# Kernel tuning notes

Hardware: AMD Instinct MI355X
Metric: run time of the kernel (lower is better)

Reference implementation:

```python
import jax, jax.numpy as jnp
import numpy as np

N = 100000; NFEAT = 256; NHID = 128; NCLASS = 40; DEG = 16; E = N * DEG
L = 2; AH = 16; ALPHA = 0.2; LP_ALPHA = 0.5


def setup_inputs() -> dict:
    key = jax.random.key(0)
    ks = jax.random.split(key, 12)
    s = 0.05
    x = jax.random.normal(ks[0], (N, NFEAT), jnp.float32)
    row = jnp.repeat(jnp.arange(N), DEG)                       # each node has DEG out-edges
    col = jax.random.randint(ks[1], (E,), 0, N)
    edges = jnp.stack([row, col])                              # [2, E]
    degree = jax.random.uniform(ks[2], (N, 1), jnp.float32, 0.5, 1.5)
    label = jax.random.uniform(ks[3], (N, NCLASS), jnp.float32)
    return {
        "x": x, "edges": edges, "degree": degree, "iftrain": 0, "label": label,
        "lb_w": jax.random.normal(ks[4], (NHID, NFEAT)) * s,
        "lb_b": jnp.zeros((NHID,)),
        "L2F": jax.random.normal(ks[5], (NCLASS, NHID)) * s,
        "Ws": jax.random.normal(ks[6], (L, 2 * NHID, NHID)) * s,
        "w2m": jax.random.normal(ks[7], (L, AH, NHID)) * s,
        "b2m": jnp.zeros((L, AH)),
        "ab": jnp.zeros((L, 1, AH + 1)),
        "lf1w": jax.random.normal(ks[8], (L, AH, (AH + 1) * 3)) * s,
        "lf1b": jnp.zeros((L, AH)),
        "lf2w": jax.random.normal(ks[9], (L, 1, AH)) * s,
        "lf2b": jnp.zeros((L, 1)),
        "LPW": jnp.ones((L, N, 1)),
        "la2w": jax.random.normal(ks[10], (NCLASS, NHID)) * s,
        "la2b": jnp.zeros((NCLASS,)),
    }


def _seg(vals, row, n):
    return jax.ops.segment_sum(vals, row, num_segments=n)


def _layer(x, pre_label, aggr, row, col, degree, lpw, W, w2m, b2m, ab, lf1w, lf1b, lf2w, lf2b):
    n = x.shape[0]
    # final_h = aggr * spmm(adj, LP_W*h*deg) * deg + (1-aggr) * h
    h = jnp.concatenate([x, pre_label], axis=1) @ W            # [N, nhid]
    agg = _seg((lpw * h * degree)[col], row, n)
    h = aggr * agg * degree + (1.0 - aggr) * h
    rowcnt = _seg(jnp.ones((row.shape[0], 1), x.dtype), row, n)  # [N,1] edges per row

    def mini(feat):
        m = feat @ w2m.T + b2m                                 # [N, AH]
        avg = _seg(m[col], row, n) / rowcnt                    # mean neighbor feature
        dist = jnp.sqrt(jnp.sum((avg[row] - m[col]) ** 2, -1) + 1e-12)  # [E]
        d2 = (_seg(dist, row, n) / rowcnt[:, 0])[:, None]      # row-wise mean distance
        return jnp.concatenate([m, d2], axis=1)                # [N, AH+1]

    def factor(hs, hd, hdiff):
        f = jnp.tanh(jnp.concatenate([hs, hd, hdiff], 1) @ lf1w.T + lf1b)
        return jax.nn.sigmoid((f @ lf2w.T + lf2b)[:, 0])       # [E]

    m0 = mini(h)
    hs0, hd0 = m0[row], m0[col]
    hdiff = jnp.abs(hd0 - hs0)
    f0 = factor(hs0, hd0, hdiff)
    m1 = mini(x)
    f1 = factor(m1[row] + ab, m1[col] + ab, hdiff)             # note: reuses hdiff (as in torch code)
    f1hop = (_seg(f1, row, n) / rowcnt[:, 0])[:, None]         # mean-reduce spmm
    f2hop = (_seg(f0 * f1hop[col, 0], row, n) / rowcnt[:, 0])[:, None]
    return jax.nn.leaky_relu(h, ALPHA), f2hop


def reference(x, edges, degree, iftrain, label, lb_w, lb_b, L2F, Ws, w2m, b2m, ab,
              lf1w, lf1b, lf2w, lf2b, LPW, la2w, la2b):
    row, col = edges[0], edges[1]
    h = x @ lb_w.T + lb_b
    pre_label = label @ L2F
    aggr = jnp.asarray(LP_ALPHA, h.dtype)
    for l in range(L):
        h, aggr = _layer(h, pre_label, aggr, row, col, degree, LPW[l], Ws[l],
                         w2m[l], b2m[l], ab[l], lf1w[l], lf1b[l], lf2w[l], lf2b[l])
    return jax.nn.log_softmax(h @ la2w.T + la2b, axis=-1)
```

## Files before the change

### kernel.cpp

```cpp
#include <hip/hip_runtime.h>
#include <hip/hip_bf16.h>
#include <hip/hip_fp8.h>
#include <math.h>

#define NN 100000
#define NCLS 40
#define DEGC 16
#define NEDGE (NN*DEGC)
#define ALPHAC 0.2f
#define LPALPHA 0.5f

typedef short short8v __attribute__((ext_vector_type(8)));
typedef float f32x4 __attribute__((ext_vector_type(4)));

__device__ __forceinline__ short f2bf(float f) {
    unsigned u = __float_as_uint(f);
    u += 0x7fff + ((u >> 16) & 1);
    return (short)(u >> 16);
}
__device__ __forceinline__ float bf2f(ushort u) {
    return __uint_as_float(((unsigned)u) << 16);
}
__device__ __forceinline__ unsigned char f2e4m3(float f) {
    __hip_fp8_e4m3 e(f);
    return (unsigned char)e.__x;
}
__device__ __forceinline__ void e4m3x4(unsigned u, float* o) {
#pragma unroll
    for (int s = 0; s < 4; ++s) {
        __hip_fp8_e4m3 e;
        e.__x = (__hip_fp8_storage_t)((u >> (8 * s)) & 0xff);
        o[s] = (float)e;
    }
}

template <int NCH1, bool ABF, bool HASL, bool WRT8, bool HASM1>
__global__ __launch_bounds__(256) void gemm128_lds(
    const void* __restrict__ A1v, const ushort* __restrict__ B1t,
    const ushort* __restrict__ labB64, const ushort* __restrict__ B2t,
    const float* __restrict__ bias, const float* __restrict__ biasm1,
    int leakyA, ushort* __restrict__ C,
    unsigned char* __restrict__ T8, ushort* __restrict__ M1out)
{
    constexpr int K1 = NCH1 * 32;
    constexpr int NG = NCH1 / 4;
    constexpr int NCH = NCH1 + (HASL ? 2 : 0);
    constexpr int BROWS = HASM1 ? 144 : 128;
    constexpr int NSLOT = BROWS / 16;
    __shared__ __align__(16) ushort Bs1[BROWS * 128];
    __shared__ __align__(16) ushort Bs2[HASL ? 128 * 64 : 8];

    const int tid = threadIdx.x;
    const int l   = tid & 63;
    const int w   = tid >> 6;
    const int lr  = l & 15;
    const int lk8 = (l >> 4) << 3;
    const int n0  = blockIdx.x * 64 + w * 16;
    int r = n0 + lr; r = r < NN ? r : NN - 1;
    const int swz = (lr & 7) << 4;

    short8v afr[NCH];
    if (ABF) {
        const ushort* __restrict__ A = (const ushort*)A1v;
#pragma unroll
        for (int kc = 0; kc < NCH1; ++kc)
            afr[kc] = *(const short8v*)(A + (size_t)r * K1 + kc * 32 + lk8);
    } else {
        const float* __restrict__ A = (const float*)A1v;
#pragma unroll
        for (int g = 0; g < NCH1; g += 2) {
            const float* p0 = A + (size_t)r * K1 + g * 32 + lk8;
            const float* p1 = A + (size_t)r * K1 + (g + 1) * 32 + lk8;
            float4 a0 = *(const float4*)p0;
            float4 a1 = *(const float4*)(p0 + 4);
            float4 b0 = *(const float4*)p1;
            float4 b1 = *(const float4*)(p1 + 4);
            short8v va, vb;
            va[0] = f2bf(a0.x); va[1] = f2bf(a0.y); va[2] = f2bf(a0.z); va[3] = f2bf(a0.w);
            va[4] = f2bf(a1.x); va[5] = f2bf(a1.y); va[6] = f2bf(a1.z); va[7] = f2bf(a1.w);
            vb[0] = f2bf(b0.x); vb[1] = f2bf(b0.y); vb[2] = f2bf(b0.z); vb[3] = f2bf(b0.w);
            vb[4] = f2bf(b1.x); vb[5] = f2bf(b1.y); vb[6] = f2bf(b1.z); vb[7] = f2bf(b1.w);
            afr[g] = va;
            afr[g + 1] = vb;
        }
    }
    if (HASL) {
        afr[NCH1]     = *(const short8v*)(labB64 + (size_t)r * 64 + lk8);
        afr[NCH1 + 1] = *(const short8v*)(labB64 + (size_t)r * 64 + 32 + lk8);
    }

    if (HASL) {
#pragma unroll
        for (int s = 0; s < 4; ++s) {
            const int slot = tid + s * 256;
            const int row = slot >> 3, colq = slot & 7;
            uint4 v = *(const uint4*)(B2t + (size_t)row * 64 + colq * 8);
            *(uint4*)((char*)Bs2 + ((row * 128 + colq * 16) ^ ((row & 7) << 4))) = v;
        }
    }

    f32x4 acc[8];
#pragma unroll
    for (int ni = 0; ni < 8; ++ni) acc[ni] = (f32x4){0.f, 0.f, 0.f, 0.f};
    f32x4 accm1 = (f32x4){0.f, 0.f, 0.f, 0.f};

#pragma unroll
    for (int g = 0; g < NG; ++g) {
        if (g) __syncthreads();
#pragma unroll
        for (int s = 0; s < NSLOT; ++s) {
            const int slot = tid + s * 256;
            const int row = slot >> 4, colq = slot & 15;
            uint4 v = *(const uint4*)(B1t + (size_t)row * K1 + g * 128 + colq * 8);
            *(uint4*)((char*)Bs1 + ((row * 256 + colq * 16) ^ ((row & 7) << 4))) = v;
        }
        __syncthreads();
        if (HASM1) {
#pragma unroll
            for (int kc = 0; kc < 4; ++kc) {
                short8v b = *(const short8v*)((const char*)Bs1 +
                    (((128 + lr) * 256 + kc * 64 + lk8 * 2) ^ swz));
                accm1 = __builtin_amdgcn_mfma_f32_16x16x32_bf16(
                    afr[g * 4 + kc], b, accm1, 0, 0, 0);
            }
        }
        if (ABF && leakyA && g == 0) {
#pragma unroll
            for (int kc = 0; kc < NCH1; ++kc)
#pragma unroll
                for (int j = 0; j < 8; ++j) {
                    float f = bf2f((ushort)afr[kc][j]);
                    f = f > 0.f ? f : ALPHAC * f;
                    afr[kc][j] = f2bf(f);
                }
        }
#pragma unroll
        for (int ni = 0; ni < 8; ++ni) {
#pragma unroll
            for (int kc = 0; kc < 4; ++kc) {
                short8v b = *(const short8v*)((const char*)Bs1 +
                    (((ni * 16 + lr) * 256 + kc * 64 + lk8 * 2) ^ swz));
                acc[ni] = __builtin_amdgcn_mfma_f32_16x16x32_bf16(afr[g * 4 + kc], b, acc[ni], 0, 0, 0);
            }
        }
    }
    if (HASL) {
#pragma unroll
        for (int ni = 0; ni < 8; ++ni) {
#pragma unroll
            for (int kc = 0; kc < 2; ++kc) {
                short8v b = *(const short8v*)((const char*)Bs2 +
                    (((ni * 16 + lr) * 128 + kc * 64 + lk8 * 2) ^ swz));
                acc[ni] = __builtin_amdgcn_mfma_f32_16x16x32_bf16(afr[NCH1 + kc], b, acc[ni], 0, 0, 0);
            }
        }
    }

    const int rsub = (l >> 4) << 2;
#pragma unroll
    for (int ni = 0; ni < 8; ++ni) {
        const int cc = ni * 16 + lr;
        const float bv = bias ? bias[cc] : 0.f;
#pragma unroll
        for (int rg = 0; rg < 4; ++rg) {
            const int rr = n0 + rsub + rg;
            if (rr < NN) {
                const float v = acc[ni][rg] + bv;
                C[(size_t)rr * 128 + cc] = (ushort)f2bf(v);
                if (WRT8) T8[(size_t)rr * 128 + cc] = f2e4m3(v);
            }
        }
    }
    if (HASM1) {
        const float bm = biasm1[lr];
#pragma unroll
        for (int rg = 0; rg < 4; ++rg) {
            const int rr = n0 + rsub + rg;
            if (rr < NN)
                M1out[(size_t)rr * 32 + lr] = (ushort)f2bf(accm1[rg] + bm);
        }
    }
}

__global__ __launch_bounds__(256) void agg_v5(
    const unsigned char* __restrict__ T8, const ushort* __restrict__ hlin,
    const int* __restrict__ col, const float* __restrict__ sd,
    const float* __restrict__ degree, const float* __restrict__ aggrv,
    const float aggrs, int do_leaky, ushort* __restrict__ hout)
{
    const int lane = threadIdx.x & 63;
    const int node = blockIdx.x * 4 + (threadIdx.x >> 6);
    const int q  = lane >> 4;
    const int cq = lane & 15;

    int cl = 0; float sl = 0.f;
    if (lane < 16) {
        cl = col[node * 16 + lane];
        sl = sd[cl];
    }

    float ax[8];
#pragma unroll
    for (int s = 0; s < 8; ++s) ax[s] = 0.f;

#pragma unroll
    for (int g = 0; g < 4; ++g) {
        const int nb = g * 4 + q;
        const int   c  = __shfl(cl, nb, 64);
        const float wv = __shfl(sl, nb, 64);
        const uint2 u = *(const uint2*)(T8 + (size_t)c * 128 + cq * 8);
        float d0[4], d1[4];
        e4m3x4(u.x, d0);
        e4m3x4(u.y, d1);
#pragma unroll
        for (int s2 = 0; s2 < 4; ++s2) {
            ax[s2]     += wv * d0[s2];
            ax[4 + s2] += wv * d1[s2];
        }
    }
#pragma unroll
    for (int s = 0; s < 8; ++s) {
        ax[s] += __shfl_xor(ax[s], 16, 64);
        ax[s] += __shfl_xor(ax[s], 32, 64);
    }

    const uint4 us = *(const uint4*)(hlin + (size_t)node * 128 + cq * 8);
    const unsigned uus[4] = {us.x, us.y, us.z, us.w};
    const float a = aggrv ? aggrv[node] : aggrs;
    const float d = degree[node];
    uint4 uo;
    unsigned* uop = &uo.x;
#pragma unroll
    for (int s = 0; s < 4; ++s) {
        float ox = a * ax[(s < 2 ? s * 2 : (s - 2) * 2 + 4)] * d;
        float oy = a * ax[(s < 2 ? s * 2 + 1 : (s - 2) * 2 + 5)] * d;
        ox += (1.f - a) * bf2f((ushort)(uus[s] & 0xffff));
        oy += (1.f - a) * bf2f((ushort)(uus[s] >> 16));
        if (do_leaky) {
            ox = ox > 0.f ? ox : ALPHAC * ox;
            oy = oy > 0.f ? oy : ALPHAC * oy;
        }
        uop[s] = (unsigned)(ushort)f2bf(ox) | ((unsigned)(ushort)f2bf(oy) << 16);
    }
    if (q == 0)
        *(uint4*)(hout + (size_t)node * 128 + cq * 8) = uo;
}

__global__ __launch_bounds__(256) void mini2_dual(
    const ushort* __restrict__ Mb01, const int* __restrict__ col,
    float* __restrict__ d2_0, float* __restrict__ d2_1)
{
    __shared__ float sm0[16][16][17];
    __shared__ float sm1[16][16][17];
    __shared__ float av0[16][16];
    __shared__ float av1[16][16];
    const int tid = threadIdx.x;
    const int g = tid >> 4, j = tid & 15;
    const int node = blockIdx.x * 16 + g;
    const int c = col[node * 16 + j];
    const ushort* __restrict__ rowp = Mb01 + (size_t)c * 32;
    const uint4 u0 = *(const uint4*)rowp;
    const uint4 u1 = *(const uint4*)(rowp + 8);
    const uint4 u2 = *(const uint4*)(rowp + 16);
    const uint4 u3 = *(const uint4*)(rowp + 24);
    const unsigned w0[8] = {u0.x, u0.y, u0.z, u0.w, u1.x, u1.y, u1.z, u1.w};
    const unsigned w1[8] = {u2.x, u2.y, u2.z, u2.w, u3.x, u3.y, u3.z, u3.w};
#pragma unroll
    for (int s = 0; s < 8; ++s) {
        sm0[g][j][s * 2]     = bf2f((ushort)(w0[s] & 0xffff));
        sm0[g][j][s * 2 + 1] = bf2f((ushort)(w0[s] >> 16));
        sm1[g][j][s * 2]     = bf2f((ushort)(w1[s] & 0xffff));
        sm1[g][j][s * 2 + 1] = bf2f((ushort)(w1[s] >> 16));
    }
    __syncthreads();
    float a0 = 0.f, a1 = 0.f;
#pragma unroll
    for (int nb = 0; nb < 16; ++nb) { a0 += sm0[g][nb][j]; a1 += sm1[g][nb][j]; }
    av0[g][j] = a0 * (1.f / 16.f);
    av1[g][j] = a1 * (1.f / 16.f);
    __syncthreads();
    float dd0 = 1e-12f, dd1 = 1e-12f;
#pragma unroll
    for (int d = 0; d < 16; ++d) {
        float t0 = av0[g][d] - sm0[g][j][d];
        float t1 = av1[g][d] - sm1[g][j][d];
        dd0 += t0 * t0;
        dd1 += t1 * t1;
    }
    float dist0 = sqrtf(dd0), dist1 = sqrtf(dd1);
#pragma unroll
    for (int off = 1; off < 16; off <<= 1) {
        dist0 += __shfl_xor(dist0, off, 64);
        dist1 += __shfl_xor(dist1, off, 64);
    }
    if (j == 0) {
        d2_0[node] = dist0 * (1.f / 16.f);
        d2_1[node] = dist1 * (1.f / 16.f);
    }
}

__global__ __launch_bounds__(256) void prep_pnode(
    const ushort* __restrict__ Mb01, const float* __restrict__ d2_0,
    const float* __restrict__ d2_1,
    const float* __restrict__ ab, const float* __restrict__ lf1w,
    const float* __restrict__ lf1b,
    float* __restrict__ P0s, float* __restrict__ P1s,
    unsigned char* __restrict__ PK8)
{
    const int idx = blockIdx.x * 256 + threadIdx.x;
    const int i = idx >> 4, k = idx & 15;
    float m0[17], m1a[17];
    const ushort* r0 = Mb01 + (size_t)i * 32;
    const ushort* r1 = r0 + 16;
#pragma unroll
    for (int d = 0; d < 16; ++d) {
        m0[d]  = bf2f(r0[d]);
        m1a[d] = bf2f(r1[d]) + ab[d];
    }
    m0[16]  = d2_0[i];
    m1a[16] = d2_1[i] + ab[16];
    const float* __restrict__ Wk = lf1w + k * 51;
    float p0s = lf1b[k], p1s = p0s, p0d = 0.f, p1d = 0.f;
#pragma unroll
    for (int d = 0; d < 17; ++d) {
        const float w0 = Wk[d], w1 = Wk[17 + d];
        p0s += m0[d]  * w0;  p0d += m0[d]  * w1;
        p1s += m1a[d] * w0;  p1d += m1a[d] * w1;
    }
    P0s[idx] = p0s;
    P1s[idx] = p1s;
    unsigned char* __restrict__ pk = PK8 + (size_t)i * 64;
    pk[k]      = f2e4m3(m0[k]);
    pk[16 + k] = f2e4m3(p0d);
    pk[32 + k] = f2e4m3(p1d);
    if (k == 0) *(float*)(pk + 48) = d2_0[i];
}

__global__ __launch_bounds__(256) void fact2_kernel(
    const unsigned char* __restrict__ PK8,
    const float* __restrict__ P0s, const float* __restrict__ P1s,
    const int* __restrict__ col,
    const float* __restrict__ W2c, const float* __restrict__ lf2w,
    const float* __restrict__ lf2b,
    float* __restrict__ f0out, float* __restrict__ f1hout)
{
    const int e = blockIdx.x * 256 + threadIdx.x;
    const int i = e >> 4;
    const int c = col[e];

    const unsigned char* __restrict__ pki = PK8 + (size_t)i * 64;
    const unsigned char* __restrict__ pkc = PK8 + (size_t)c * 64;
    const uint4 mi8 = *(const uint4*)pki;
    const float d2i = *(const float*)(pki + 48);
    const uint4 mc8 = *(const uint4*)pkc;
    const uint4 p08 = *(const uint4*)(pkc + 16);
    const uint4 p18 = *(const uint4*)(pkc + 32);
    const float d2c = *(const float*)(pkc + 48);

    float mi[16], mc[16], P0d[16], P1d[16];
    e4m3x4(mi8.x, mi);     e4m3x4(mi8.y, mi + 4);
    e4m3x4(mi8.z, mi + 8); e4m3x4(mi8.w, mi + 12);
    e4m3x4(mc8.x, mc);     e4m3x4(mc8.y, mc + 4);
    e4m3x4(mc8.z, mc + 8); e4m3x4(mc8.w, mc + 12);
    e4m3x4(p08.x, P0d);     e4m3x4(p08.y, P0d + 4);
    e4m3x4(p08.z, P0d + 8); e4m3x4(p08.w, P0d + 12);
    e4m3x4(p18.x, P1d);     e4m3x4(p18.y, P1d + 4);
    e4m3x4(p18.z, P1d + 8); e4m3x4(p18.w, P1d + 12);

    float2 H2[8];
#pragma unroll
    for (int k2 = 0; k2 < 8; ++k2) H2[k2] = make_float2(0.f, 0.f);
#pragma unroll
    for (int d = 0; d < 16; ++d) {
        const float hd = fabsf(mc[d] - mi[d]);
        const float2* __restrict__ wv = (const float2*)(W2c + d * 16);
#pragma unroll
        for (int k2 = 0; k2 < 8; ++k2) {
            H2[k2].x = fmaf(hd, wv[k2].x, H2[k2].x);
            H2[k2].y = fmaf(hd, wv[k2].y, H2[k2].y);
        }
    }
    {
        const float hdd = fabsf(d2c - d2i);
        const float2* __restrict__ wv = (const float2*)(W2c + 16 * 16);
#pragma unroll
        for (int k2 = 0; k2 < 8; ++k2) {
            H2[k2].x = fmaf(hdd, wv[k2].x, H2[k2].x);
            H2[k2].y = fmaf(hdd, wv[k2].y, H2[k2].y);
        }
    }
    const float* __restrict__ H = (const float*)H2;

    const float* __restrict__ p0 = P0s + (size_t)i * 16;
    const float* __restrict__ p1 = P1s + (size_t)i * 16;
    float a0 = lf2b[0], a1 = a0;
#pragma unroll
    for (int k = 0; k < 16; ++k) {
        const float t0 = p0[k] + P0d[k] + H[k];
        const float t1 = p1[k] + P1d[k] + H[k];
        const float lw = lf2w[k];
        a0 += (1.f - 2.f / (__expf(2.f * t0) + 1.f)) * lw;
        a1 += (1.f - 2.f / (__expf(2.f * t1) + 1.f)) * lw;
    }
    f0out[e] = 1.f / (1.f + __expf(-a0));
    float f1 = 1.f / (1.f + __expf(-a1));
#pragma unroll
    for (int off = 1; off < 16; off <<= 1) f1 += __shfl_xor(f1, off, 64);
    if ((threadIdx.x & 15) == 0) f1hout[i] = f1 * (1.f / 16.f);
}

__global__ void f2hop_kernel(const float* __restrict__ f0, const float* __restrict__ f1h,
                             const int* __restrict__ col, float* __restrict__ out)
{
    const int i = blockIdx.x * 256 + threadIdx.x;
    if (i >= NN) return;
    float s = 0.f;
#pragma unroll
    for (int t = 0; t < 16; ++t) {
        int e = i * 16 + t;
        s += f0[e] * f1h[col[e]];
    }
    out[i] = s * (1.f / 16.f);
}

__global__ __launch_bounds__(256) void logits_mfma(
    const ushort* __restrict__ X, const ushort* __restrict__ Wb48,
    const float* __restrict__ bias, float* __restrict__ out)
{
    __shared__ __align__(16) ushort Wl[48 * 128];
    const int tid = threadIdx.x;
    const int l  = tid & 63;
    const int w  = tid >> 6;
    const int lr = l & 15;
    const int lk = (l >> 4) << 3;
    const int swz = (lr & 7) << 4;
#pragma unroll
    for (int s = 0; s < 6; ++s) {
        const int slot = tid + s * 256;
        const int row = slot >> 4, colq = slot & 15;
        uint4 v = *(const uint4*)(Wb48 + (size_t)row * 128 + colq * 8);
        *(uint4*)((char*)Wl + ((row * 256 + colq * 16) ^ ((row & 7) << 4))) = v;
    }
    const int row_base = blockIdx.x * 128 + w * 32;
    short8v afr[2][4];
#pragma unroll
    for (int mi = 0; mi < 2; ++mi) {
        int r = row_base + mi * 16 + lr;
        r = r < NN ? r : NN - 1;
#pragma unroll
        for (int kc = 0; kc < 4; ++kc)
            afr[mi][kc] = *(const short8v*)(X + (size_t)r * 128 + kc * 32 + lk);
    }
    __syncthreads();
    f32x4 acc[2][3];
#pragma unroll
    for (int mi = 0; mi < 2; ++mi)
#pragma unroll
        for (int ni = 0; ni < 3; ++ni) acc[mi][ni] = (f32x4){0.f, 0.f, 0.f, 0.f};
#pragma unroll
    for (int ni = 0; ni < 3; ++ni) {
#pragma unroll
        for (int kc = 0; kc < 4; ++kc) {
            short8v b = *(const short8v*)((const char*)Wl +
                (((ni * 16 + lr) * 256 + kc * 64 + lk * 2) ^ swz));
#pragma unroll
            for (int mi = 0; mi < 2; ++mi)
                acc[mi][ni] = __builtin_amdgcn_mfma_f32_16x16x32_bf16(afr[mi][kc], b, acc[mi][ni], 0, 0, 0);
        }
    }

    const float b0 = bias[lr];
    const float b1 = bias[16 + lr];
    const float b2 = (lr < 8) ? bias[32 + lr] : 0.f;
    const int rsub = (l >> 4) << 2;
#pragma unroll
    for (int mi = 0; mi < 2; ++mi) {
#pragma unroll
        for (int reg = 0; reg < 4; ++reg) {
            const int row = row_base + mi * 16 + rsub + reg;
            const float z0 = acc[mi][0][reg] + b0;
            const float z1 = acc[mi][1][reg] + b1;
            const float z2 = (lr < 8) ? acc[mi][2][reg] + b2 : -1e30f;
            float m = fmaxf(fmaxf(z0, z1), z2);
#pragma unroll
            for (int off = 1; off < 16; off <<= 1) m = fmaxf(m, __shfl_xor(m, off, 64));
            float s = __expf(z0 - m) + __expf(z1 - m) + ((lr < 8) ? __expf(z2 - m) : 0.f);
#pragma unroll
            for (int off = 1; off < 16; off <<= 1) s += __shfl_xor(s, off, 64);
            const float lg = m + __logf(s);
            if (row < NN) {
                float* __restrict__ po = out + (size_t)row * NCLS;
                po[lr] = z0 - lg;
                po[16 + lr] = z1 - lg;
                if (lr < 8) po[32 + lr] = z2 - lg;
            }
        }
    }
}

__global__ void prep_misc(
    const float* __restrict__ lb_w, const float* __restrict__ lb_b,
    const float* __restrict__ Ws, ushort* __restrict__ WtL1,
    const float* __restrict__ L2F, ushort* __restrict__ W2t,
    const float* __restrict__ la2w, ushort* __restrict__ Wb48,
    const float* __restrict__ lf1w, float* __restrict__ W2c,
    const float* __restrict__ w2m, const float* __restrict__ b2m,
    const float* __restrict__ LPW, const float* __restrict__ degree,
    float* __restrict__ sd2, ushort* __restrict__ B1x,
    float* __restrict__ bias1, float* __restrict__ bm1e)
{
    int b = blockIdx.x;
    const int tid = threadIdx.x;
    if (b < 64) {
        int i = b * 256 + tid;
        int m = i >> 7, k = i & 127;
        WtL1[(size_t)m * 128 + k] = (ushort)f2bf(Ws[32768 + (size_t)k * 128 + m]);
        return;
    }
    b -= 64;
    if (b < 16) {
        int i = b * 256 + tid;
        WtL1[128 * 128 + i] = (ushort)f2bf(w2m[i]);
        return;
    }
    b -= 16;
    if (b < 64) {
        int i = b * 256 + tid;
        int ll = i >> 13, r = i & 8191;
        int m = r >> 6, c = r & 63;
        float acc = 0.f;
        if (c < NCLS) {
            const float* Wl = Ws + (size_t)ll * 32768 + 128 * 128;
            for (int j = 0; j < 128; ++j) acc += L2F[c * 128 + j] * Wl[j * 128 + m];
        }
        W2t[i] = (ushort)f2bf(acc);
        return;
    }
    b -= 64;
    if (b < 24) {
        int i = b * 256 + tid;
        if (i < 48 * 128) {
            int c = i >> 7;
            Wb48[i] = (c < NCLS) ? (ushort)f2bf(la2w[i]) : (ushort)0;
        }
        return;
    }
    b -= 24;
    if (b < 2) {
        int t = b * 256 + tid;
        if (t < 272) {
            int d = t >> 4, k = t & 15;
            W2c[t] = lf1w[k * 51 + 34 + d];
        }
        return;
    }
    b -= 2;
    if (b < 391) {
        int i = b * 256 + tid;
        if (i < NN) sd2[i] = LPW[i] * degree[i];
        return;
    }
    b -= 391;
    if (b < 391) {
        int i = b * 256 + tid;
        if (i < NN) sd2[NN + i] = LPW[NN + i] * degree[i];
        return;
    }
    b -= 391;
    if (b < 128) {
        int i = b * 256 + tid;
        int m = i >> 8, k = i & 255;
        float acc = 0.f;
        for (int mp = 0; mp < 128; ++mp)
            acc += lb_w[mp * 256 + k] * Ws[mp * 128 + m];
        B1x[(size_t)m * 256 + k] = (ushort)f2bf(acc);
        return;
    }
    b -= 128;
    if (b < 16) {
        int i = b * 256 + tid;
        int j = i >> 8, k = i & 255;
        float acc = 0.f;
        for (int mp = 0; mp < 128; ++mp)
            acc += lb_w[mp * 256 + k] * w2m[j * 128 + mp];
        B1x[(size_t)(128 + j) * 256 + k] = (ushort)f2bf(acc);
        return;
    }
    b -= 16;
    {
        if (tid < 128) {
            float acc = 0.f;
            for (int mp = 0; mp < 128; ++mp) acc += lb_b[mp] * Ws[mp * 128 + tid];
            bias1[tid] = acc;
        } else if (tid < 144) {
            const int j = tid - 128;
            float acc = b2m[j];
            for (int mp = 0; mp < 128; ++mp) acc += lb_b[mp] * w2m[j * 128 + mp];
            bm1e[j] = acc;
        }
    }
}

__global__ void cvt_label64v(const float* __restrict__ label, ushort* __restrict__ labB64)
{
    const int idx = blockIdx.x * 256 + threadIdx.x;
    const int i = idx >> 4;
    const int c0 = (idx & 15) * 4;
    ushort o[4];
#pragma unroll
    for (int j = 0; j < 4; ++j) {
        const int c = c0 + j;
        o[j] = (c < NCLS) ? (ushort)f2bf(label[(size_t)i * NCLS + c]) : (ushort)0;
    }
    *(uint2*)(labB64 + (size_t)i * 64 + c0) = make_uint2(
        (unsigned)o[0] | ((unsigned)o[1] << 16),
        (unsigned)o[2] | ((unsigned)o[3] << 16));
}

extern "C" void kernel_launch(void* const* d_in, const int* in_sizes, int n_in,
                              void* d_out, int out_size, void* d_ws, size_t ws_size,
                              hipStream_t stream)
{
    const float* x      = (const float*)d_in[0];
    const int*   edges  = (const int*)d_in[1];
    const float* degree = (const float*)d_in[2];
    const float* label  = (const float*)d_in[4];
    const float* lb_w   = (const float*)d_in[5];
    const float* lb_b   = (const float*)d_in[6];
    const float* L2F    = (const float*)d_in[7];
    const float* Ws     = (const float*)d_in[8];
    const float* w2m    = (const float*)d_in[9];
    const float* b2m    = (const float*)d_in[10];
    const float* ab     = (const float*)d_in[11];
    const float* lf1w   = (const float*)d_in[12];
    const float* lf1b   = (const float*)d_in[13];
    const float* lf2w   = (const float*)d_in[14];
    const float* lf2b   = (const float*)d_in[15];
    const float* LPW    = (const float*)d_in[16];
    const float* la2w   = (const float*)d_in[17];
    const float* la2b   = (const float*)d_in[18];
    const int* colp = edges + NEDGE;

    float* ws = (float*)d_ws;
    size_t o = 0;
    float* d2_0B = ws + o; o += NN;
    float* d2_1B = ws + o; o += NN;
    float* P0sB  = ws + o; o += (size_t)NN * 16;
    float* P1sB  = ws + o; o += (size_t)NN * 16;
    float* f0B   = ws + o; o += NEDGE;
    float* f1hB  = ws + o; o += NN;
    float* aggrB = ws + o; o += NN;
    float* sd2B  = ws + o; o += 2 * NN;
    float* W2cB  = ws + o; o += 272;
    float* bias1B = ws + o; o += 128;
    float* bm1eB  = ws + o; o += 16;
    ushort* bufA = (ushort*)(ws + o); o += (size_t)NN * 128 / 2;
    ushort* bufL = (ushort*)(ws + o); o += (size_t)NN * 128 / 2;
    ushort* labB64 = (ushort*)(ws + o); o += (size_t)NN * 64 / 2;
    ushort* Mb01 = (ushort*)(ws + o); o += (size_t)NN * 32 / 2;
    unsigned char* PK8 = (unsigned char*)(ws + o); o += (size_t)NN * 64 / 4;
    ushort* B1x  = (ushort*)(ws + o); o += 144 * 256 / 2;
    ushort* WtL1 = (ushort*)(ws + o); o += 144 * 128 / 2;
    ushort* W2t  = (ushort*)(ws + o); o += 2 * 128 * 64 / 2;
    ushort* Wb48 = (ushort*)(ws + o); o += 48 * 128 / 2;
    unsigned char* T8 = (unsigned char*)(ws + o); o += (size_t)NN * 128 / 4;

    dim3 b256(256);
    prep_misc<<<1097, b256, 0, stream>>>(lb_w, lb_b, Ws, WtL1, L2F, W2t, la2w, Wb48,
                                         lf1w, W2cB, w2m, b2m, LPW, degree,
                                         sd2B, B1x, bias1B, bm1eB);
    cvt_label64v<<<6250, b256, 0, stream>>>(label, labB64);

    gemm128_lds<8, false, true, true, true><<<1563, b256, 0, stream>>>(
        x, B1x, labB64, W2t, bias1B, bm1eB, 0, bufL, T8, Mb01 + 16);
    agg_v5<<<25000, b256, 0, stream>>>(T8, bufL, colp, sd2B, degree,
                                       nullptr, LPALPHA, 0, bufA);

    gemm128_lds<4, true, true, true, true><<<1563, b256, 0, stream>>>(
        bufA, WtL1, labB64, W2t + 8192, nullptr, b2m, 1, bufL, T8, Mb01);

    mini2_dual<<<6250, b256, 0, stream>>>(Mb01, colp, d2_0B, d2_1B);
    prep_pnode<<<6250, b256, 0, stream>>>(Mb01, d2_0B, d2_1B, ab, lf1w, lf1b,
                                          P0sB, P1sB, PK8);
    fact2_kernel<<<6250, b256, 0, stream>>>(PK8, P0sB, P1sB, colp,
                                            W2cB, lf2w, lf2b, f0B, f1hB);
    f2hop_kernel<<<391, b256, 0, stream>>>(f0B, f1hB, colp, aggrB);

    agg_v5<<<25000, b256, 0, stream>>>(T8, bufL, colp, sd2B + NN, degree,
                                       aggrB, 0.f, 1, bufA);

    logits_mfma<<<782, b256, 0, stream>>>(bufA, Wb48, la2b, (float*)d_out);
}
```

Measured before the change: 303.2 us.

## Fuse mini2 distance and per-node prep kernels; use 512-thread GEMM blocks

Merges the neighbor-distance kernel with the per-node projection kernel, so the d2 values stay in registers and are never written to and re-read from global memory, and one launch is removed. Separately, the two GEMM kernels move to 512-thread blocks covering 128 rows each, which halves how often each block reloads the B matrix into LDS. The larger block also raises per-block register and LDS pressure, which may lower occupancy.

```diff
diff --git a/kernel.cpp b/kernel.cpp
--- a/kernel.cpp
+++ b/kernel.cpp
@@ -35,7 +35,7 @@
 }
 
 template <int NCH1, bool ABF, bool HASL, bool WRT8, bool HASM1>
-__global__ __launch_bounds__(256) void gemm128_lds(
+__global__ __launch_bounds__(512) void gemm128_lds(
     const void* __restrict__ A1v, const ushort* __restrict__ B1t,
     const ushort* __restrict__ labB64, const ushort* __restrict__ B2t,
     const float* __restrict__ bias, const float* __restrict__ biasm1,
@@ -46,7 +46,7 @@
     constexpr int NG = NCH1 / 4;
     constexpr int NCH = NCH1 + (HASL ? 2 : 0);
     constexpr int BROWS = HASM1 ? 144 : 128;
-    constexpr int NSLOT = BROWS / 16;
+    constexpr int TOTSLOT = BROWS * 16;
     __shared__ __align__(16) ushort Bs1[BROWS * 128];
     __shared__ __align__(16) ushort Bs2[HASL ? 128 * 64 : 8];
 
@@ -55,7 +55,7 @@
     const int w   = tid >> 6;
     const int lr  = l & 15;
     const int lk8 = (l >> 4) << 3;
-    const int n0  = blockIdx.x * 64 + w * 16;
+    const int n0  = blockIdx.x * 128 + w * 16;
     int r = n0 + lr; r = r < NN ? r : NN - 1;
     const int swz = (lr & 7) << 4;
 
@@ -91,8 +91,8 @@
 
     if (HASL) {
 #pragma unroll
-        for (int s = 0; s < 4; ++s) {
-            const int slot = tid + s * 256;
+        for (int s = 0; s < 2; ++s) {
+            const int slot = tid + s * 512;
             const int row = slot >> 3, colq = slot & 7;
             uint4 v = *(const uint4*)(B2t + (size_t)row * 64 + colq * 8);
             *(uint4*)((char*)Bs2 + ((row * 128 + colq * 16) ^ ((row & 7) << 4))) = v;
@@ -108,11 +108,13 @@
     for (int g = 0; g < NG; ++g) {
         if (g) __syncthreads();
 #pragma unroll
-        for (int s = 0; s < NSLOT; ++s) {
-            const int slot = tid + s * 256;
-            const int row = slot >> 4, colq = slot & 15;
-            uint4 v = *(const uint4*)(B1t + (size_t)row * K1 + g * 128 + colq * 8);
-            *(uint4*)((char*)Bs1 + ((row * 256 + colq * 16) ^ ((row & 7) << 4))) = v;
+        for (int s = 0; s < (TOTSLOT + 511) / 512; ++s) {
+            const int slot = tid + s * 512;
+            if (slot < TOTSLOT) {
+                const int row = slot >> 4, colq = slot & 15;
+                uint4 v = *(const uint4*)(B1t + (size_t)row * K1 + g * 128 + colq * 8);
+                *(uint4*)((char*)Bs1 + ((row * 256 + colq * 16) ^ ((row & 7) << 4))) = v;
+            }
         }
         __syncthreads();
         if (HASM1) {
@@ -246,9 +248,12 @@
         *(uint4*)(hout + (size_t)node * 128 + cq * 8) = uo;
 }
 
-__global__ __launch_bounds__(256) void mini2_dual(
+__global__ __launch_bounds__(256) void mini2p(
     const ushort* __restrict__ Mb01, const int* __restrict__ col,
-    float* __restrict__ d2_0, float* __restrict__ d2_1)
+    const float* __restrict__ ab, const float* __restrict__ lf1w,
+    const float* __restrict__ lf1b,
+    float* __restrict__ P0s, float* __restrict__ P1s,
+    unsigned char* __restrict__ PK8)
 {
     __shared__ float sm0[16][16][17];
     __shared__ float sm1[16][16][17];
@@ -293,22 +298,10 @@
         dist0 += __shfl_xor(dist0, off, 64);
         dist1 += __shfl_xor(dist1, off, 64);
     }
-    if (j == 0) {
-        d2_0[node] = dist0 * (1.f / 16.f);
-        d2_1[node] = dist1 * (1.f / 16.f);
-    }
-}
-
-__global__ __launch_bounds__(256) void prep_pnode(
-    const ushort* __restrict__ Mb01, const float* __restrict__ d2_0,
-    const float* __restrict__ d2_1,
-    const float* __restrict__ ab, const float* __restrict__ lf1w,
-    const float* __restrict__ lf1b,
-    float* __restrict__ P0s, float* __restrict__ P1s,
-    unsigned char* __restrict__ PK8)
-{
-    const int idx = blockIdx.x * 256 + threadIdx.x;
-    const int i = idx >> 4, k = idx & 15;
+    const float d2_0 = dist0 * (1.f / 16.f);
+    const float d2_1 = dist1 * (1.f / 16.f);
+
+    const int i = node, k = j;
     float m0[17], m1a[17];
     const ushort* r0 = Mb01 + (size_t)i * 32;
     const ushort* r1 = r0 + 16;
@@ -317,23 +310,24 @@
         m0[d]  = bf2f(r0[d]);
         m1a[d] = bf2f(r1[d]) + ab[d];
     }
-    m0[16]  = d2_0[i];
-    m1a[16] = d2_1[i] + ab[16];
+    m0[16]  = d2_0;
+    m1a[16] = d2_1 + ab[16];
     const float* __restrict__ Wk = lf1w + k * 51;
     float p0s = lf1b[k], p1s = p0s, p0d = 0.f, p1d = 0.f;
 #pragma unroll
     for (int d = 0; d < 17; ++d) {
-        const float w0 = Wk[d], w1 = Wk[17 + d];
-        p0s += m0[d]  * w0;  p0d += m0[d]  * w1;
-        p1s += m1a[d] * w0;  p1d += m1a[d] * w1;
-    }
+        const float w0v = Wk[d], w1v = Wk[17 + d];
+        p0s += m0[d]  * w0v;  p0d += m0[d]  * w1v;
+        p1s += m1a[d] * w0v;  p1d += m1a[d] * w1v;
+    }
+    const int idx = i * 16 + k;
     P0s[idx] = p0s;
     P1s[idx] = p1s;
     unsigned char* __restrict__ pk = PK8 + (size_t)i * 64;
     pk[k]      = f2e4m3(m0[k]);
     pk[16 + k] = f2e4m3(p0d);
     pk[32 + k] = f2e4m3(p1d);
-    if (k == 0) *(float*)(pk + 48) = d2_0[i];
+    if (k == 0) *(float*)(pk + 48) = d2_0;
 }
 
 __global__ __launch_bounds__(256) void fact2_kernel(
@@ -643,8 +637,6 @@
 
     float* ws = (float*)d_ws;
     size_t o = 0;
-    float* d2_0B = ws + o; o += NN;
-    float* d2_1B = ws + o; o += NN;
     float* P0sB  = ws + o; o += (size_t)NN * 16;
     float* P1sB  = ws + o; o += (size_t)NN * 16;
     float* f0B   = ws + o; o += NEDGE;
@@ -666,22 +658,21 @@
     unsigned char* T8 = (unsigned char*)(ws + o); o += (size_t)NN * 128 / 4;
 
     dim3 b256(256);
+    dim3 b512(512);
     prep_misc<<<1097, b256, 0, stream>>>(lb_w, lb_b, Ws, WtL1, L2F, W2t, la2w, Wb48,
                                          lf1w, W2cB, w2m, b2m, LPW, degree,
                                          sd2B, B1x, bias1B, bm1eB);
     cvt_label64v<<<6250, b256, 0, stream>>>(label, labB64);
 
-    gemm128_lds<8, false, true, true, true><<<1563, b256, 0, stream>>>(
+    gemm128_lds<8, false, true, true, true><<<782, b512, 0, stream>>>(
         x, B1x, labB64, W2t, bias1B, bm1eB, 0, bufL, T8, Mb01 + 16);
     agg_v5<<<25000, b256, 0, stream>>>(T8, bufL, colp, sd2B, degree,
                                        nullptr, LPALPHA, 0, bufA);
 
-    gemm128_lds<4, true, true, true, true><<<1563, b256, 0, stream>>>(
+    gemm128_lds<4, true, true, true, true><<<782, b512, 0, stream>>>(
         bufA, WtL1, labB64, W2t + 8192, nullptr, b2m, 1, bufL, T8, Mb01);
 
-    mini2_dual<<<6250, b256, 0, stream>>>(Mb01, colp, d2_0B, d2_1B);
-    prep_pnode<<<6250, b256, 0, stream>>>(Mb01, d2_0B, d2_1B, ab, lf1w, lf1b,
-                                          P0sB, P1sB, PK8);
+    mini2p<<<6250, b256, 0, stream>>>(Mb01, colp, ab, lf1w, lf1b, P0sB, P1sB, PK8);
     fact2_kernel<<<6250, b256, 0, stream>>>(PK8, P0sB, P1sB, colp,
                                             W2cB, lf2w, lf2b, f0B, f1hB);
     f2hop_kernel<<<391, b256, 0, stream>>>(f0B, f1hB, colp, aggrB);
```

After: 306.1 us. Within noise of the previous version (+1.0%).
